# Kernel optimization log

Hardware: AMD Instinct MI355X
Metric: run time of the kernel (lower is better)

Reference implementation:

```python
import jax, jax.numpy as jnp
import numpy as np

N, E, R, B, IN, H, OUT, P = 20000, 320000, 8, 8, 128, 256, 128, 100000
LN_EPS = 1e-5


def _xavier(key, shape):
    fan_in, fan_out = shape[-2], shape[-1]
    lim = float(np.sqrt(6.0 / (fan_in + fan_out)))
    return jax.random.uniform(key, shape, jnp.float32, -lim, lim)


def setup_inputs() -> dict:
    key = jax.random.key(0)
    ks = iter(jax.random.split(key, 64))
    inp = {}
    inp['x'] = jax.random.normal(next(ks), (N, IN), jnp.float32)
    inp['edge_index'] = jax.random.randint(next(ks), (2, E), 0, N, jnp.int32)
    inp['edge_type'] = jax.random.randint(next(ks), (E,), 0, R, jnp.int32)
    inp['gene_pairs'] = jax.random.randint(next(ks), (2, P), 0, N, jnp.int32)
    dims = [(IN, H), (H, H), (H, H), (H, OUT)]  # per-layer (in_ch, out_ch)
    for i, (ic, oc) in enumerate(dims):
        inp[f'basis{i}'] = _xavier(next(ks), (B, ic, oc))
        inp[f'att{i}'] = _xavier(next(ks), (R, B))
        inp[f'root{i}'] = _xavier(next(ks), (ic, oc))
        inp[f'relatt{i}'] = jnp.ones((R,), jnp.float32)
        inp[f'g{i}'] = jnp.ones((oc,), jnp.float32)
        inp[f'b{i}'] = jnp.zeros((oc,), jnp.float32)
    inp['res0'] = _xavier(next(ks), (IN, H))   # in_ch != out_ch at layer 0
    inp['res3'] = _xavier(next(ks), (H, OUT))  # and at layer 3
    # decoder: 3*OUT -> H -> H//2 -> H//4 -> 1
    ddims = [(3 * OUT, H), (H, H // 2), (H // 2, H // 4), (H // 4, 1)]
    for i, (ic, oc) in enumerate(ddims):
        inp[f'dW{i}'] = _xavier(next(ks), (ic, oc))
        inp[f'db{i}'] = jnp.zeros((oc,), jnp.float32)
        if i < 3:
            inp[f'dg{i}'] = jnp.ones((oc,), jnp.float32)
            inp[f'dbb{i}'] = jnp.zeros((oc,), jnp.float32)
    return inp


def _ln(h, g, b):
    m = h.mean(-1, keepdims=True)
    v = ((h - m) ** 2).mean(-1, keepdims=True)
    return (h - m) * jax.lax.rsqrt(v + LN_EPS) * g + b


def _conv(x, src, dst, et, basis, att, root_w, rel_att):
    # W_r = sum_b att[r,b] * B_b ; message = a_{r(e)} * x_src @ W_{r(e)}
    # Since the message is linear, aggregate x_src per (dst, relation) first
    # (segment_sum), then apply the R small GEMMs once - same math, no [E,in,out].
    n, d = x.shape
    weight = jnp.einsum('rb,bio->rio', att, basis)          # [R,in,out]
    a = jax.nn.softmax(rel_att)                              # [R]
    seg = dst.astype(jnp.int32) * R + et.astype(jnp.int32)   # [(node,rel)] segment ids
    agg = jax.ops.segment_sum(x[src], seg, num_segments=n * R).reshape(n, R, d)
    out = jnp.einsum('nri,rio->no', agg, weight * a[:, None, None])
    return out + x @ root_w


def reference(x, edge_index, edge_type, gene_pairs,
              basis0, att0, root0, relatt0, g0, b0, res0,
              basis1, att1, root1, relatt1, g1, b1,
              basis2, att2, root2, relatt2, g2, b2,
              basis3, att3, root3, relatt3, g3, b3, res3,
              dW0, db0, dg0, dbb0, dW1, db1, dg1, dbb1,
              dW2, db2, dg2, dbb2, dW3, db3):
    src, dst = edge_index[0], edge_index[1]
    layers = [
        (basis0, att0, root0, relatt0, g0, b0, res0),
        (basis1, att1, root1, relatt1, g1, b1, None),
        (basis2, att2, root2, relatt2, g2, b2, None),
        (basis3, att3, root3, relatt3, g3, b3, res3),
    ]
    h = x
    for i, (bs, at, rt, ra, g, b, res) in enumerate(layers):
        h_in = h
        h = _conv(h, src, dst, edge_type, bs, at, rt, ra)
        h = _ln(h, g, b)
        h = h + (h_in @ res if res is not None else h_in)
        if i < len(layers) - 1:
            h = jax.nn.gelu(h, approximate=False)
    z = h  # [N, OUT]
    zi, zj = z[gene_pairs[0]], z[gene_pairs[1]]
    pe = jnp.concatenate([zi + zj, zi * zj, jnp.abs(zi - zj)], axis=-1)
    d = jax.nn.gelu(_ln(pe @ dW0 + db0, dg0, dbb0), approximate=False)
    d = jax.nn.gelu(_ln(d @ dW1 + db1, dg1, dbb1), approximate=False)
    d = jax.nn.gelu(_ln(d @ dW2 + db2, dg2, dbb2), approximate=False)
    logits = (d @ dW3 + db3).squeeze(-1)  # [P]
    return logits, z
```

## Files before the change

kernel.cpp:

```cpp
#include <hip/hip_runtime.h>
#include <hip/hip_bf16.h>
#include <math.h>
#include <cstddef>
#include <stdint.h>

#define NN 20000
#define EE 320000
#define RR 8
#define PP 100000
#define NR (NN * RR)

typedef __hip_bfloat16 bf16;
typedef __attribute__((ext_vector_type(8))) short short8;
typedef __attribute__((ext_vector_type(4))) short short4v;
typedef __attribute__((ext_vector_type(4))) float floatx4;

__device__ __forceinline__ float b2f(bf16 v) { return __bfloat162float(v); }
__device__ __forceinline__ bf16 f2b(float v) { return __float2bfloat16(v); }
__device__ __forceinline__ float bits2f(unsigned short u) {
  unsigned int i = ((unsigned int)u) << 16; float f; __builtin_memcpy(&f, &i, 4); return f;
}
__device__ __forceinline__ short f2bits(float f) {
  bf16 h = __float2bfloat16(f); short s; __builtin_memcpy(&s, &h, 2); return s;
}
__device__ __forceinline__ float gelu_f(float x) {
  float t = x * (0.7978845608f + 0.0356774081f * x * x);
  float s = exp2f(-2.885390082f * t);
  return x * __builtin_amdgcn_rcpf(1.f + s);
}
__device__ __forceinline__ void async_copy16(void* lds, const void* g) {
  __builtin_amdgcn_global_load_lds((const __attribute__((address_space(1))) void*)g,
                                   (__attribute__((address_space(3))) void*)lds, 16, 0, 0);
}
__device__ __forceinline__ const short8* frag_at(const bf16* base, int row, int q) {
  return (const short8*)(base + row * 64 + (((q) ^ (row & 7)) << 3));
}
__device__ __forceinline__ const short8* frag256(const bf16* base, int row, int col64, int q) {
  return (const short8*)(base + row * 256 + col64 + (((q) ^ (row & 7)) << 3));
}
__device__ __forceinline__ int idx128(int row, int qg) {
  return row * 128 + ((qg >> 3) << 6) + (((qg & 7) ^ (row & 7)) << 3);
}

__global__ void hist_k(const int* __restrict__ dst, const int* __restrict__ et,
                       int* __restrict__ counts) {
  int e = blockIdx.x * 256 + threadIdx.x;
  if (e >= EE) return;
  atomicAdd(&counts[dst[e] * RR + et[e]], 1);
}

__global__ void scan1_k(const int* __restrict__ counts, int* __restrict__ prefix,
                        int* __restrict__ bsums) {
  __shared__ int tmp[256];
  int i = blockIdx.x * 256 + threadIdx.x;
  int v = counts[i];
  tmp[threadIdx.x] = v; __syncthreads();
  for (int off = 1; off < 256; off <<= 1) {
    int x = (threadIdx.x >= off) ? tmp[threadIdx.x - off] : 0;
    __syncthreads();
    tmp[threadIdx.x] += x;
    __syncthreads();
  }
  prefix[i] = tmp[threadIdx.x] - v;
  if (threadIdx.x == 255) bsums[blockIdx.x] = tmp[255];
}

__global__ void scan2_k(int* __restrict__ bsums, int nb) {
  __shared__ int tmp[256];
  __shared__ int carry;
  if (threadIdx.x == 0) carry = 0;
  __syncthreads();
  for (int base = 0; base < nb; base += 256) {
    int i = base + threadIdx.x;
    int v = (i < nb) ? bsums[i] : 0;
    tmp[threadIdx.x] = v; __syncthreads();
    for (int off = 1; off < 256; off <<= 1) {
      int x = (threadIdx.x >= off) ? tmp[threadIdx.x - off] : 0;
      __syncthreads();
      tmp[threadIdx.x] += x;
      __syncthreads();
    }
    int c = carry;
    if (i < nb) bsums[i] = c + tmp[threadIdx.x] - v;
    __syncthreads();
    if (threadIdx.x == 255) carry = c + tmp[255];
    __syncthreads();
  }
}

__global__ void scan3_k(int* __restrict__ prefix, const int* __restrict__ bsums) {
  int i = blockIdx.x * 256 + threadIdx.x;
  prefix[i] += bsums[blockIdx.x];
}

__global__ void scatter_k(const int* __restrict__ src, const int* __restrict__ dst,
                          const int* __restrict__ et, const int* __restrict__ segstart,
                          int* __restrict__ cursor, int* __restrict__ ssrc) {
  int e = blockIdx.x * 256 + threadIdx.x;
  if (e >= EE) return;
  int s = dst[e] * RR + et[e];
  int pos = atomicAdd(&cursor[s], 1);
  ssrc[segstart[s] + pos] = src[e];
}

__global__ void cvt_bf16_k(const float* __restrict__ in, bf16* __restrict__ out, int n) {
  int i = blockIdx.x * 256 + threadIdx.x;
  if (i < n) out[i] = f2b(in[i]);
}

__global__ void softmax4_k(const float* r0, const float* r1, const float* r2,
                           const float* r3, float* __restrict__ a) {
  if (threadIdx.x == 0) {
    const float* rs[4] = {r0, r1, r2, r3};
    for (int l = 0; l < 4; ++l) {
      float mx = -1e30f;
      for (int i = 0; i < RR; ++i) mx = fmaxf(mx, rs[l][i]);
      float e[RR]; float s = 0.f;
      for (int i = 0; i < RR; ++i) { e[i] = expf(rs[l][i] - mx); s += e[i]; }
      for (int i = 0; i < RR; ++i) a[l * RR + i] = e[i] / s;
    }
  }
}

__global__ void transpose_k(const float* __restrict__ in, bf16* __restrict__ out,
                            int rows, int cols) {
  int idx = blockIdx.x * 256 + threadIdx.x;
  if (idx >= rows * cols) return;
  int r = idx / cols, c = idx - r * cols;
  out[(size_t)c * rows + r] = f2b(in[idx]);
}

__global__ void prep_w_k(const float* __restrict__ basis, const float* __restrict__ att,
                         const float* __restrict__ root, const float* __restrict__ a,
                         bf16* __restrict__ Wt, int ic, int icsh, int oc, int ocsh) {
  int idx = blockIdx.x * 256 + threadIdx.x;
  int cols = 9 * ic;
  if (idx >= cols * oc) return;
  int o = idx & (oc - 1);
  int col = idx >> ocsh;
  int r = col >> icsh;
  int k = col & (ic - 1);
  float val;
  if (r < RR) {
    float acc = 0.f;
    for (int bb = 0; bb < RR; ++bb)
      acc += att[r * RR + bb] * basis[((size_t)bb * ic + k) * oc + o];
    val = a[r] * acc;
  } else {
    val = root[(size_t)k * oc + o];
  }
  Wt[(size_t)o * cols + col] = f2b(val);
}

__global__ __launch_bounds__(256) void aggregate_k(
    const bf16* __restrict__ h, const int* __restrict__ segstart,
    const int* __restrict__ counts, const int* __restrict__ ssrc,
    bf16* __restrict__ agg, int ic, int tpnsh) {
  int tpn = 1 << tpnsh;
  int npb = 256 >> tpnsh;
  int local = threadIdx.x >> tpnsh;
  int n = blockIdx.x * npb + local;
  if (n >= NN) return;
  int cbase = (threadIdx.x & (tpn - 1)) * 8;
  size_t rowoff = (size_t)n * (9 * ic);
  for (int r = 0; r < RR; ++r) {
    int s = n * RR + r;
    int st = segstart[s];
    int cnt = counts[s];
    float a[8] = {0.f, 0.f, 0.f, 0.f, 0.f, 0.f, 0.f, 0.f};
    for (int i = 0; i < cnt; ++i) {
      int src = ssrc[st + i];
      short8 v = *(const short8*)(h + (size_t)src * ic + cbase);
#pragma unroll
      for (int j = 0; j < 8; ++j) a[j] += bits2f((unsigned short)v[j]);
    }
    short8 o;
#pragma unroll
    for (int j = 0; j < 8; ++j) o[j] = f2bits(a[j]);
    *(short8*)(agg + rowoff + r * ic + cbase) = o;
  }
  *(short8*)(agg + rowoff + 8 * ic + cbase) =
      *(const short8*)(h + (size_t)n * ic + cbase);
}

__global__ __launch_bounds__(256) void gemm_f32_k(
    const bf16* __restrict__ A, const bf16* __restrict__ Wt,
    float* __restrict__ Cf, int M, int N, int K, int nb) {
  const int bid = blockIdx.x;
  const int xcd = bid & 7;
  const int slot = bid >> 3;
  const int gidx = slot / nb;
  const int member = slot - gidx * nb;
  const int mb = (M + 127) >> 7;
  const int m = gidx * 8 + xcd;
  if (m >= mb) return;
  const int m0 = m * 128;
  const int n0 = member * 64;

  __shared__ __align__(16) bf16 As[128 * 64];
  __shared__ __align__(16) bf16 Ws[64 * 64];
  const int tid = threadIdx.x;
  const int wave = tid >> 6, lane = tid & 63;
  const int quad = lane >> 4, l16 = lane & 15;
  const int wm = (wave >> 1) * 64, wn = (wave & 1) * 32;
  floatx4 acc[4][2];
#pragma unroll
  for (int i = 0; i < 4; ++i)
#pragma unroll
    for (int j = 0; j < 2; ++j) acc[i][j] = (floatx4){0.f, 0.f, 0.f, 0.f};

  for (int k0 = 0; k0 < K; k0 += 64) {
#pragma unroll
    for (int q = 0; q < 4; ++q) {
      int c0 = (wave * 4 + q) * 1024;
      int row = (c0 >> 7) + (lane >> 3);
      int grow = m0 + row; if (grow >= M) grow = M - 1;
      int ch = (lane & 7) ^ (row & 7);
      async_copy16((char*)As + c0, A + (size_t)grow * K + k0 + ch * 8);
    }
#pragma unroll
    for (int q = 0; q < 2; ++q) {
      int c0 = (wave * 2 + q) * 1024;
      int row = (c0 >> 7) + (lane >> 3);
      int ch = (lane & 7) ^ (row & 7);
      async_copy16((char*)Ws + c0, Wt + (size_t)(n0 + row) * K + k0 + ch * 8);
    }
    __syncthreads();
#pragma unroll
    for (int kk = 0; kk < 64; kk += 32) {
      int qb = (kk >> 3) + quad;
      short8 b0 = *frag_at(Ws, wn + l16, qb);
      short8 b1 = *frag_at(Ws, wn + 16 + l16, qb);
#pragma unroll
      for (int i = 0; i < 4; ++i) {
        short8 a = *frag_at(As, wm + i * 16 + l16, qb);
        acc[i][0] = __builtin_amdgcn_mfma_f32_16x16x32_bf16(a, b0, acc[i][0], 0, 0, 0);
        acc[i][1] = __builtin_amdgcn_mfma_f32_16x16x32_bf16(a, b1, acc[i][1], 0, 0, 0);
      }
    }
    __syncthreads();
  }
#pragma unroll
  for (int i = 0; i < 4; ++i)
#pragma unroll
    for (int j = 0; j < 2; ++j)
#pragma unroll
      for (int r = 0; r < 4; ++r) {
        int row = m0 + wm + i * 16 + quad * 4 + r;
        int col = n0 + wn + j * 16 + l16;
        if (row < M) Cf[(size_t)row * N + col] = acc[i][j][r];
      }
}

__global__ __launch_bounds__(256) void gemm_plain_k(
    const bf16* __restrict__ A, const bf16* __restrict__ Wt,
    bf16* __restrict__ Cb, int M, int N, int K) {
  __shared__ __align__(16) bf16 As[64 * 64];
  __shared__ __align__(16) bf16 Ws[64 * 64];
  const int m0 = blockIdx.y * 64;
  const int n0 = blockIdx.x * 64;
  const int tid = threadIdx.x;
  const int wave = tid >> 6, lane = tid & 63;
  const int quad = lane >> 4, l16 = lane & 15;
  const int wm = (wave >> 1) * 32, wn = (wave & 1) * 32;
  floatx4 acc00 = {0.f, 0.f, 0.f, 0.f};
  floatx4 acc01 = acc00, acc10 = acc00, acc11 = acc00;

  for (int k0 = 0; k0 < K; k0 += 64) {
#pragma unroll
    for (int q = 0; q < 2; ++q) {
      int c0 = (wave * 2 + q) * 1024;
      int row = (c0 >> 7) + (lane >> 3);
      int grow = m0 + row; if (grow >= M) grow = M - 1;
      int ch = (lane & 7) ^ (row & 7);
      async_copy16((char*)As + c0, A + (size_t)grow * K + k0 + ch * 8);
    }
#pragma unroll
    for (int q = 0; q < 2; ++q) {
      int c0 = (wave * 2 + q) * 1024;
      int row = (c0 >> 7) + (lane >> 3);
      int ch = (lane & 7) ^ (row & 7);
      async_copy16((char*)Ws + c0, Wt + (size_t)(n0 + row) * K + k0 + ch * 8);
    }
    __syncthreads();
#pragma unroll
    for (int kk = 0; kk < 64; kk += 32) {
      int qb = (kk >> 3) + quad;
      short8 a0 = *frag_at(As, wm + l16, qb);
      short8 a1 = *frag_at(As, wm + 16 + l16, qb);
      short8 b0 = *frag_at(Ws, wn + l16, qb);
      short8 b1 = *frag_at(Ws, wn + 16 + l16, qb);
      acc00 = __builtin_amdgcn_mfma_f32_16x16x32_bf16(a0, b0, acc00, 0, 0, 0);
      acc01 = __builtin_amdgcn_mfma_f32_16x16x32_bf16(a0, b1, acc01, 0, 0, 0);
      acc10 = __builtin_amdgcn_mfma_f32_16x16x32_bf16(a1, b0, acc10, 0, 0, 0);
      acc11 = __builtin_amdgcn_mfma_f32_16x16x32_bf16(a1, b1, acc11, 0, 0, 0);
    }
    __syncthreads();
  }
  floatx4 accs[2][2] = {{acc00, acc01}, {acc10, acc11}};
#pragma unroll
  for (int i = 0; i < 2; ++i)
#pragma unroll
    for (int j = 0; j < 2; ++j)
#pragma unroll
      for (int r = 0; r < 4; ++r) {
        int row = m0 + wm + i * 16 + quad * 4 + r;
        int col = n0 + wn + j * 16 + l16;
        if (row < M) Cb[(size_t)row * N + col] = f2b(accs[i][j][r]);
      }
}

__global__ __launch_bounds__(256) void ln_conv_k(
    const float* __restrict__ conv, const bf16* __restrict__ res,
    const float* __restrict__ g, const float* __restrict__ b,
    bf16* __restrict__ out, float* __restrict__ zout, int oc, int do_gelu) {
  int wave = threadIdx.x >> 6, lane = threadIdx.x & 63;
  int row = blockIdx.x * 4 + wave;
  if (row >= NN) return;
  int ne = oc >> 6;
  float v[4];
  float s = 0.f, s2 = 0.f;
  for (int i = 0; i < ne; ++i) {
    v[i] = conv[(size_t)row * oc + i * 64 + lane];
    s += v[i]; s2 += v[i] * v[i];
  }
  for (int off = 32; off; off >>= 1) { s += __shfl_xor(s, off); s2 += __shfl_xor(s2, off); }
  float m = s / oc;
  float var = s2 / oc - m * m;
  float rs = rsqrtf(var + 1e-5f);
  for (int i = 0; i < ne; ++i) {
    int c = i * 64 + lane;
    float y = (v[i] - m) * rs * g[c] + b[c];
    y += b2f(res[(size_t)row * oc + c]);
    if (zout) zout[(size_t)row * oc + c] = y;
    if (do_gelu) y = gelu_f(y);
    out[(size_t)row * oc + c] = f2b(y);
  }
}

__global__ __launch_bounds__(256) void gemm_pe_k(
    const bf16* __restrict__ z, const int* __restrict__ pairs,
    const bf16* __restrict__ WBT, const bf16* __restrict__ WCT,
    bf16* __restrict__ P0) {
  const int bid = blockIdx.x;
  const int xcd = bid & 7;
  const int slot = bid >> 3;
  const int gidx = slot >> 2;
  const int member = slot & 3;
  const int mb = (PP + 127) >> 7;
  const int m = gidx * 8 + xcd;
  if (m >= mb) return;
  const int m0 = m * 128;
  const int n0 = member * 64;

  __shared__ __align__(16) bf16 PEs[128 * 64];
  __shared__ __align__(16) bf16 Ws[64 * 64];
  const int tid = threadIdx.x;
  const int wave = tid >> 6, lane = tid & 63;
  const int quad = lane >> 4, l16 = lane & 15;
  const int wm = (wave >> 1) * 64, wn = (wave & 1) * 32;

  const int prow = tid >> 1;
  const int colq = (tid & 1) * 32;
  int pp = m0 + prow; if (pp >= PP) pp = PP - 1;
  const bf16* zi = z + (size_t)pairs[pp] * 128;
  const bf16* zj = z + (size_t)pairs[PP + pp] * 128;

  floatx4 acc[4][2];
#pragma unroll
  for (int i = 0; i < 4; ++i)
#pragma unroll
    for (int j = 0; j < 2; ++j) acc[i][j] = (floatx4){0.f, 0.f, 0.f, 0.f};

#pragma unroll
  for (int kwi = 0; kwi < 2; ++kwi) {
    const int kw = kwi * 64;
    short8 va[4], vb[4];
#pragma unroll
    for (int c8 = 0; c8 < 4; ++c8) {
      va[c8] = *(const short8*)(zi + kw + colq + c8 * 8);
      vb[c8] = *(const short8*)(zj + kw + colq + c8 * 8);
    }
#pragma unroll
    for (int op = 0; op < 2; ++op) {
      const bf16* W = (op == 0) ? WBT : WCT;
#pragma unroll
      for (int q = 0; q < 2; ++q) {
        int c0 = q * 4096 + wave * 1024;
        int row = (c0 >> 7) + (lane >> 3);
        int ch = (lane & 7) ^ (row & 7);
        async_copy16((char*)Ws + c0, W + (size_t)(n0 + row) * 128 + kw + ch * 8);
      }
#pragma unroll
      for (int c8 = 0; c8 < 4; ++c8) {
        short8 o;
#pragma unroll
        for (int jj = 0; jj < 8; ++jj) {
          float fa = bits2f((unsigned short)va[c8][jj]);
          float fb = bits2f((unsigned short)vb[c8][jj]);
          float v = (op == 0) ? (fa * fb) : fabsf(fa - fb);
          o[jj] = f2bits(v);
        }
        int q = (tid & 1) * 4 + c8;
        *(short8*)(PEs + prow * 64 + ((q ^ (prow & 7)) << 3)) = o;
      }
      __syncthreads();
#pragma unroll
      for (int kk = 0; kk < 64; kk += 32) {
        int qb = (kk >> 3) + quad;
        short8 b0 = *frag_at(Ws, wn + l16, qb);
        short8 b1 = *frag_at(Ws, wn + 16 + l16, qb);
#pragma unroll
        for (int i = 0; i < 4; ++i) {
          short8 a = *frag_at(PEs, wm + i * 16 + l16, qb);
          acc[i][0] = __builtin_amdgcn_mfma_f32_16x16x32_bf16(a, b0, acc[i][0], 0, 0, 0);
          acc[i][1] = __builtin_amdgcn_mfma_f32_16x16x32_bf16(a, b1, acc[i][1], 0, 0, 0);
        }
      }
      __syncthreads();
    }
  }

#pragma unroll
  for (int i = 0; i < 4; ++i)
#pragma unroll
    for (int j = 0; j < 2; ++j)
#pragma unroll
      for (int r = 0; r < 4; ++r) {
        int row = m0 + wm + i * 16 + quad * 4 + r;
        int col = n0 + wn + j * 16 + l16;
        if (row < PP) P0[(size_t)row * 256 + col] = f2b(acc[i][j][r]);
      }
}

__global__ __launch_bounds__(256) void ln_d0_k(bf16* __restrict__ D0,
                                               const int* __restrict__ pairs,
                                               const bf16* __restrict__ ZA,
                                               const float* __restrict__ db0,
                                               const float* __restrict__ g,
                                               const float* __restrict__ b) {
  int wave = threadIdx.x >> 6, lane = threadIdx.x & 63;
  int row = blockIdx.x * 4 + wave;
  if (row >= PP) return;
  int gi = pairs[row], gj = pairs[PP + row];
  bf16* p = D0 + (size_t)row * 256 + lane * 4;
  short4v xv = *(const short4v*)p;
  short4v av = *(const short4v*)(ZA + (size_t)gi * 256 + lane * 4);
  short4v bv = *(const short4v*)(ZA + (size_t)gj * 256 + lane * 4);
  float v[4];
  float s = 0.f, s2 = 0.f;
#pragma unroll
  for (int k = 0; k < 4; ++k) {
    v[k] = bits2f((unsigned short)xv[k]) + bits2f((unsigned short)av[k]) +
           bits2f((unsigned short)bv[k]) + db0[lane * 4 + k];
    s += v[k]; s2 += v[k] * v[k];
  }
  for (int off = 32; off; off >>= 1) { s += __shfl_xor(s, off); s2 += __shfl_xor(s2, off); }
  float m = s / 256.f;
  float var = s2 / 256.f - m * m;
  float rs = rsqrtf(var + 1e-5f);
  short4v ov;
#pragma unroll
  for (int k = 0; k < 4; ++k) {
    int c = lane * 4 + k;
    float y = (v[k] - m) * rs * g[c] + b[c];
    ov[k] = f2bits(gelu_f(y));
  }
  *(short4v*)p = ov;
}

__global__ __launch_bounds__(256) void lngemm1_k(
    const bf16* __restrict__ D0, const bf16* __restrict__ W1t,
    const float* __restrict__ bias, bf16* __restrict__ P1, int M) {
  __shared__ __align__(16) bf16 As[64 * 256];
  __shared__ __align__(16) bf16 Ws[128 * 64];
  const int tid = threadIdx.x;
  const int wave = tid >> 6, lane = tid & 63;
  const int quad = lane >> 4, l16 = lane & 15;
  const int wr = (wave >> 1) * 32;
  const int wc = (wave & 1) * 64;
  const int m0 = blockIdx.x * 64;

  {
    const int srow = tid >> 2;
    const int q4 = tid & 3;
    int grow = m0 + srow; if (grow >= M) grow = M - 1;
    const bf16* src = D0 + (size_t)grow * 256 + q4 * 64;
#pragma unroll
    for (int c8 = 0; c8 < 8; ++c8) {
      short8 o = *(const short8*)(src + c8 * 8);
      *(short8*)(As + srow * 256 + q4 * 64 + ((c8 ^ (srow & 7)) << 3)) = o;
    }
  }

  floatx4 acc[2][4];
#pragma unroll
  for (int i = 0; i < 2; ++i)
#pragma unroll
    for (int j = 0; j < 4; ++j) acc[i][j] = (floatx4){0.f, 0.f, 0.f, 0.f};

  for (int kc = 0; kc < 4; ++kc) {
#pragma unroll
    for (int q = 0; q < 4; ++q) {
      int c0 = q * 4096 + wave * 1024;
      int row = (c0 >> 7) + (lane >> 3);
      int ch = (lane & 7) ^ (row & 7);
      async_copy16((char*)Ws + c0, W1t + (size_t)row * 256 + kc * 64 + ch * 8);
    }
    __syncthreads();
#pragma unroll
    for (int kk = 0; kk < 64; kk += 32) {
      int qb = (kk >> 3) + quad;
      short8 a0 = *frag256(As, wr + l16, kc * 64, qb);
      short8 a1 = *frag256(As, wr + 16 + l16, kc * 64, qb);
#pragma unroll
      for (int j = 0; j < 4; ++j) {
        short8 bb = *frag_at(Ws, wc + j * 16 + l16, qb);
        acc[0][j] = __builtin_amdgcn_mfma_f32_16x16x32_bf16(a0, bb, acc[0][j], 0, 0, 0);
        acc[1][j] = __builtin_amdgcn_mfma_f32_16x16x32_bf16(a1, bb, acc[1][j], 0, 0, 0);
      }
    }
    __syncthreads();
  }

#pragma unroll
  for (int i = 0; i < 2; ++i)
#pragma unroll
    for (int r = 0; r < 4; ++r) {
      int row = wr + i * 16 + quad * 4 + r;
      int grow = m0 + row;
      if (grow >= M) continue;
#pragma unroll
      for (int j = 0; j < 4; ++j) {
        int col = wc + j * 16 + l16;
        P1[(size_t)grow * 128 + col] = f2b(acc[i][j][r] + bias[col]);
      }
    }
}

__global__ __launch_bounds__(256) void lngemm2_k(
    const bf16* __restrict__ P1, const bf16* __restrict__ W2t,
    const float* __restrict__ g, const float* __restrict__ b,
    const float* __restrict__ bias, bf16* __restrict__ P2, int M) {
  __shared__ __align__(16) bf16 As[64 * 128];
  __shared__ __align__(16) bf16 Ws[64 * 64];
  const int tid = threadIdx.x;
  const int wave = tid >> 6, lane = tid & 63;
  const int quad = lane >> 4, l16 = lane & 15;
  const int m0 = blockIdx.x * 64;

  {
    const int srow = tid >> 2;
    const int q4 = tid & 3;
    int grow = m0 + srow; if (grow >= M) grow = M - 1;
    const bf16* src = P1 + (size_t)grow * 128 + q4 * 32;
    float v[32];
    float s = 0.f, s2 = 0.f;
#pragma unroll
    for (int c8 = 0; c8 < 4; ++c8) {
      short8 x = *(const short8*)(src + c8 * 8);
#pragma unroll
      for (int jj = 0; jj < 8; ++jj) {
        float f = bits2f((unsigned short)x[jj]);
        v[c8 * 8 + jj] = f; s += f; s2 += f * f;
      }
    }
    s += __shfl_xor(s, 1); s2 += __shfl_xor(s2, 1);
    s += __shfl_xor(s, 2); s2 += __shfl_xor(s2, 2);
    float mean = s / 128.f;
    float var = s2 / 128.f - mean * mean;
    float rs = rsqrtf(var + 1e-5f);
#pragma unroll
    for (int c8 = 0; c8 < 4; ++c8) {
      short8 o;
#pragma unroll
      for (int jj = 0; jj < 8; ++jj) {
        int col = q4 * 32 + c8 * 8 + jj;
        float y = (v[c8 * 8 + jj] - mean) * rs * g[col] + b[col];
        o[jj] = f2bits(gelu_f(y));
      }
      *(short8*)(As + idx128(srow, q4 * 4 + c8)) = o;
    }
  }

  floatx4 acc[4];
#pragma unroll
  for (int j = 0; j < 4; ++j) acc[j] = (floatx4){0.f, 0.f, 0.f, 0.f};

  for (int kc = 0; kc < 2; ++kc) {
#pragma unroll
    for (int q = 0; q < 2; ++q) {
      int c0 = q * 4096 + wave * 1024;
      int row = (c0 >> 7) + (lane >> 3);
      int ch = (lane & 7) ^ (row & 7);
      async_copy16((char*)Ws + c0, W2t + (size_t)row * 128 + kc * 64 + ch * 8);
    }
    __syncthreads();
#pragma unroll
    for (int kk = 0; kk < 64; kk += 32) {
      int qb = (kk >> 3) + quad;
      short8 a = *(const short8*)(As + idx128(wave * 16 + l16, kc * 8 + qb));
#pragma unroll
      for (int j = 0; j < 4; ++j) {
        short8 bb = *frag_at(Ws, j * 16 + l16, qb);
        acc[j] = __builtin_amdgcn_mfma_f32_16x16x32_bf16(a, bb, acc[j], 0, 0, 0);
      }
    }
    __syncthreads();
  }

#pragma unroll
  for (int r = 0; r < 4; ++r) {
    int row = wave * 16 + quad * 4 + r;
    int grow = m0 + row;
    if (grow >= M) continue;
#pragma unroll
    for (int j = 0; j < 4; ++j) {
      int col = j * 16 + l16;
      P2[(size_t)grow * 64 + col] = f2b(acc[j][r] + bias[col]);
    }
  }
}

__global__ __launch_bounds__(256) void logits_k(const bf16* __restrict__ P2,
                                                const float* __restrict__ g,
                                                const float* __restrict__ b,
                                                const float* __restrict__ w3,
                                                const float* __restrict__ b3,
                                                float* __restrict__ out) {
  int wave = threadIdx.x >> 6, lane = threadIdx.x & 63;
  int p = blockIdx.x * 4 + wave;
  if (p >= PP) return;
  float v = b2f(P2[(size_t)p * 64 + lane]);
  float s = v, s2 = v * v;
  for (int off = 32; off; off >>= 1) { s += __shfl_xor(s, off); s2 += __shfl_xor(s2, off); }
  float m = s / 64.f;
  float var = s2 / 64.f - m * m;
  float rs = rsqrtf(var + 1e-5f);
  float y = gelu_f((v - m) * rs * g[lane] + b[lane]);
  float t = y * w3[lane];
  for (int off = 32; off; off >>= 1) t += __shfl_xor(t, off);
  if (lane == 0) out[p] = t + b3[0];
}

extern "C" void kernel_launch(void* const* d_in, const int* in_sizes, int n_in,
                              void* d_out, int out_size, void* d_ws, size_t ws_size,
                              hipStream_t stream) {
  auto cdiv = [](int a, int b) { return (a + b - 1) / b; };

  const float* x = (const float*)d_in[0];
  const int* ei = (const int*)d_in[1];
  const int* et = (const int*)d_in[2];
  const int* gp = (const int*)d_in[3];
  const float *basis[4], *att[4], *root[4], *relatt[4], *gln[4], *bln[4];
  for (int l = 0; l < 4; ++l) {
    basis[l]  = (const float*)d_in[4 + 6 * l];
    att[l]    = (const float*)d_in[5 + 6 * l];
    root[l]   = (const float*)d_in[6 + 6 * l];
    relatt[l] = (const float*)d_in[7 + 6 * l];
    gln[l]    = (const float*)d_in[8 + 6 * l];
    bln[l]    = (const float*)d_in[9 + 6 * l];
  }
  const float* res0 = (const float*)d_in[28];
  const float* res3 = (const float*)d_in[29];
  const float* dW0 = (const float*)d_in[30]; const float* db0 = (const float*)d_in[31];
  const float* dg0 = (const float*)d_in[32]; const float* dbb0 = (const float*)d_in[33];
  const float* dW1 = (const float*)d_in[34]; const float* db1 = (const float*)d_in[35];
  const float* dg1 = (const float*)d_in[36]; const float* dbb1 = (const float*)d_in[37];
  const float* dW2 = (const float*)d_in[38]; const float* db2 = (const float*)d_in[39];
  const float* dg2 = (const float*)d_in[40]; const float* dbb2 = (const float*)d_in[41];
  const float* dW3 = (const float*)d_in[42]; const float* db3 = (const float*)d_in[43];

  char* base = (char*)d_ws;
  size_t off = 0;
  auto alloc = [&](size_t bytes) -> char* {
    char* p = base + off;
    off += (bytes + 255) & ~(size_t)255;
    return p;
  };
  bf16* X16 = (bf16*)alloc((size_t)NN * 128 * 2);
  bf16* HA  = (bf16*)alloc((size_t)NN * 256 * 2);
  bf16* HB  = (bf16*)alloc((size_t)NN * 256 * 2);
  bf16* RESB = (bf16*)alloc((size_t)NN * 256 * 2);
  bf16* ZA   = (bf16*)alloc((size_t)NN * 256 * 2);
  float* CONV = (float*)alloc((size_t)NN * 256 * 4);
  bf16* WT    = (bf16*)alloc((size_t)589824 * 2);
  bf16* RES0T = (bf16*)alloc((size_t)32768 * 2);
  bf16* RES3T = (bf16*)alloc((size_t)32768 * 2);
  bf16* WAT   = (bf16*)alloc((size_t)32768 * 2);
  bf16* WBT   = (bf16*)alloc((size_t)32768 * 2);
  bf16* WCT   = (bf16*)alloc((size_t)32768 * 2);
  bf16* DW1T  = (bf16*)alloc((size_t)32768 * 2);
  bf16* DW2T  = (bf16*)alloc((size_t)8192 * 2);
  float* ASOFT = (float*)alloc(32 * 4);
  int* COUNTS = (int*)alloc((size_t)NR * 4);
  int* SEG    = (int*)alloc((size_t)NR * 4);
  int* CUR    = (int*)alloc((size_t)NR * 4);
  int* BS     = (int*)alloc(1024 * 4);
  int* SSRC   = (int*)alloc((size_t)EE * 4);
  char* BIG = alloc(93000000);
  bf16* AGG = (bf16*)BIG;
  bf16* D0  = (bf16*)BIG;
  bf16* P1  = (bf16*)alloc((size_t)PP * 128 * 2);
  bf16* P2  = (bf16*)alloc((size_t)PP * 64 * 2);
  (void)ws_size; (void)in_sizes; (void)n_in; (void)out_size;

  float* out_logits = (float*)d_out;
  float* out_z = (float*)d_out + PP;

  hipMemsetAsync(COUNTS, 0, (size_t)NR * 4, stream);
  hipMemsetAsync(CUR, 0, (size_t)NR * 4, stream);
  hist_k<<<cdiv(EE, 256), 256, 0, stream>>>(ei + EE, et, COUNTS);
  scan1_k<<<NR / 256, 256, 0, stream>>>(COUNTS, SEG, BS);
  scan2_k<<<1, 256, 0, stream>>>(BS, NR / 256);
  scan3_k<<<NR / 256, 256, 0, stream>>>(SEG, BS);
  scatter_k<<<cdiv(EE, 256), 256, 0, stream>>>(ei, ei + EE, et, SEG, CUR, SSRC);

  cvt_bf16_k<<<cdiv(NN * 128, 256), 256, 0, stream>>>(x, X16, NN * 128);
  softmax4_k<<<1, 64, 0, stream>>>(relatt[0], relatt[1], relatt[2], relatt[3], ASOFT);
  transpose_k<<<cdiv(128 * 256, 256), 256, 0, stream>>>(res0, RES0T, 128, 256);
  transpose_k<<<cdiv(256 * 128, 256), 256, 0, stream>>>(res3, RES3T, 256, 128);
  transpose_k<<<cdiv(128 * 256, 256), 256, 0, stream>>>(dW0, WAT, 128, 256);
  transpose_k<<<cdiv(128 * 256, 256), 256, 0, stream>>>(dW0 + 128 * 256, WBT, 128, 256);
  transpose_k<<<cdiv(128 * 256, 256), 256, 0, stream>>>(dW0 + 256 * 256, WCT, 128, 256);
  transpose_k<<<cdiv(256 * 128, 256), 256, 0, stream>>>(dW1, DW1T, 256, 128);
  transpose_k<<<cdiv(128 * 64, 256), 256, 0, stream>>>(dW2, DW2T, 128, 64);

  const int mb = cdiv(NN, 128);
  const int swzP4 = 8 * cdiv(mb, 8) * 4;
  const int swzP2 = 8 * cdiv(mb, 8) * 2;

  prep_w_k<<<cdiv(9 * 128 * 256, 256), 256, 0, stream>>>(basis[0], att[0], root[0], ASOFT + 0, WT, 128, 7, 256, 8);
  aggregate_k<<<cdiv(NN, 16), 256, 0, stream>>>(X16, SEG, COUNTS, SSRC, AGG, 128, 4);
  gemm_plain_k<<<dim3(4, cdiv(NN, 64)), 256, 0, stream>>>(X16, RES0T, RESB, NN, 256, 128);
  gemm_f32_k<<<swzP4, 256, 0, stream>>>(AGG, WT, CONV, NN, 256, 1152, 4);
  ln_conv_k<<<cdiv(NN, 4), 256, 0, stream>>>(CONV, RESB, gln[0], bln[0], HA, nullptr, 256, 1);

  prep_w_k<<<cdiv(9 * 256 * 256, 256), 256, 0, stream>>>(basis[1], att[1], root[1], ASOFT + 8, WT, 256, 8, 256, 8);
  aggregate_k<<<cdiv(NN, 8), 256, 0, stream>>>(HA, SEG, COUNTS, SSRC, AGG, 256, 5);
  gemm_f32_k<<<swzP4, 256, 0, stream>>>(AGG, WT, CONV, NN, 256, 2304, 4);
  ln_conv_k<<<cdiv(NN, 4), 256, 0, stream>>>(CONV, HA, gln[1], bln[1], HB, nullptr, 256, 1);

  prep_w_k<<<cdiv(9 * 256 * 256, 256), 256, 0, stream>>>(basis[2], att[2], root[2], ASOFT + 16, WT, 256, 8, 256, 8);
  aggregate_k<<<cdiv(NN, 8), 256, 0, stream>>>(HB, SEG, COUNTS, SSRC, AGG, 256, 5);
  gemm_f32_k<<<swzP4, 256, 0, stream>>>(AGG, WT, CONV, NN, 256, 2304, 4);
  ln_conv_k<<<cdiv(NN, 4), 256, 0, stream>>>(CONV, HB, gln[2], bln[2], HA, nullptr, 256, 1);

  prep_w_k<<<cdiv(9 * 256 * 128, 256), 256, 0, stream>>>(basis[3], att[3], root[3], ASOFT + 24, WT, 256, 8, 128, 7);
  aggregate_k<<<cdiv(NN, 8), 256, 0, stream>>>(HA, SEG, COUNTS, SSRC, AGG, 256, 5);
  gemm_plain_k<<<dim3(2, cdiv(NN, 64)), 256, 0, stream>>>(HA, RES3T, RESB, NN, 128, 256);
  gemm_f32_k<<<swzP2, 256, 0, stream>>>(AGG, WT, CONV, NN, 128, 2304, 2);
  ln_conv_k<<<cdiv(NN, 4), 256, 0, stream>>>(CONV, RESB, gln[3], bln[3], HB, out_z, 128, 0);

  gemm_plain_k<<<dim3(4, cdiv(NN, 64)), 256, 0, stream>>>(HB, WAT, ZA, NN, 256, 128);
  const int pb = cdiv(PP, 128);
  const int swzPE = 8 * cdiv(pb, 8) * 4;
  gemm_pe_k<<<swzPE, 256, 0, stream>>>(HB, gp, WBT, WCT, D0);
  ln_d0_k<<<cdiv(PP, 4), 256, 0, stream>>>(D0, gp, ZA, db0, dg0, dbb0);
  lngemm1_k<<<cdiv(PP, 64), 256, 0, stream>>>(D0, DW1T, db1, P1, PP);
  lngemm2_k<<<cdiv(PP, 4 * 16), 256, 0, stream>>>(P1, DW2T, dg1, dbb1, db2, P2, PP);
  logits_k<<<cdiv(PP, 4), 256, 0, stream>>>(P2, dg2, dbb2, dW3, db3, out_logits);
}
```

Baseline: 762.0 us.

## Fuse decoder layer-0 LayerNorm into GEMM1 load and interleave aggregation relations

The separate ln_d0_k pass is removed. Its bias add, ZA gathers, LayerNorm and GELU now run while lngemm1_k loads its A tile, with four threads per row reducing the statistics through shuffles. This avoids a full read and write of the 100000x256 D0 buffer and one kernel launch, at the cost of 64 floats of register state per thread. The aggregate kernel also loads segment starts and counts as vectors and walks two relations at once, unrolled by two, so more independent gathers are in flight.

```diff
diff --git a/kernel.cpp b/kernel.cpp
--- a/kernel.cpp
+++ b/kernel.cpp
@@ -14,6 +14,7 @@
 typedef __attribute__((ext_vector_type(8))) short short8;
 typedef __attribute__((ext_vector_type(4))) short short4v;
 typedef __attribute__((ext_vector_type(4))) float floatx4;
+typedef __attribute__((ext_vector_type(4))) int intx4;
 
 __device__ __forceinline__ float b2f(bf16 v) { return __bfloat162float(v); }
 __device__ __forceinline__ bf16 f2b(float v) { return __float2bfloat16(v); }
@@ -163,21 +164,69 @@
   if (n >= NN) return;
   int cbase = (threadIdx.x & (tpn - 1)) * 8;
   size_t rowoff = (size_t)n * (9 * ic);
-  for (int r = 0; r < RR; ++r) {
-    int s = n * RR + r;
-    int st = segstart[s];
-    int cnt = counts[s];
-    float a[8] = {0.f, 0.f, 0.f, 0.f, 0.f, 0.f, 0.f, 0.f};
-    for (int i = 0; i < cnt; ++i) {
-      int src = ssrc[st + i];
-      short8 v = *(const short8*)(h + (size_t)src * ic + cbase);
-#pragma unroll
-      for (int j = 0; j < 8; ++j) a[j] += bits2f((unsigned short)v[j]);
-    }
-    short8 o;
-#pragma unroll
-    for (int j = 0; j < 8; ++j) o[j] = f2bits(a[j]);
-    *(short8*)(agg + rowoff + r * ic + cbase) = o;
+  const bf16* hc = h + cbase;
+
+  intx4 stv0 = *(const intx4*)(segstart + n * RR);
+  intx4 stv1 = *(const intx4*)(segstart + n * RR + 4);
+  intx4 ctv0 = *(const intx4*)(counts + n * RR);
+  intx4 ctv1 = *(const intx4*)(counts + n * RR + 4);
+  int sts[8] = {stv0[0], stv0[1], stv0[2], stv0[3], stv1[0], stv1[1], stv1[2], stv1[3]};
+  int cts[8] = {ctv0[0], ctv0[1], ctv0[2], ctv0[3], ctv1[0], ctv1[1], ctv1[2], ctv1[3]};
+
+#pragma unroll
+  for (int rp = 0; rp < 4; ++rp) {
+    const int stA = sts[rp],     cA = cts[rp];
+    const int stB = sts[rp + 4], cB = cts[rp + 4];
+    float aA[8] = {0.f, 0.f, 0.f, 0.f, 0.f, 0.f, 0.f, 0.f};
+    float aB[8] = {0.f, 0.f, 0.f, 0.f, 0.f, 0.f, 0.f, 0.f};
+    int iA = 0, iB = 0;
+    while (iA + 2 <= cA && iB + 2 <= cB) {
+      int sA0 = ssrc[stA + iA], sA1 = ssrc[stA + iA + 1];
+      int sB0 = ssrc[stB + iB], sB1 = ssrc[stB + iB + 1];
+      short8 vA0 = *(const short8*)(hc + (size_t)sA0 * ic);
+      short8 vA1 = *(const short8*)(hc + (size_t)sA1 * ic);
+      short8 vB0 = *(const short8*)(hc + (size_t)sB0 * ic);
+      short8 vB1 = *(const short8*)(hc + (size_t)sB1 * ic);
+#pragma unroll
+      for (int j = 0; j < 8; ++j) {
+        aA[j] += bits2f((unsigned short)vA0[j]) + bits2f((unsigned short)vA1[j]);
+        aB[j] += bits2f((unsigned short)vB0[j]) + bits2f((unsigned short)vB1[j]);
+      }
+      iA += 2; iB += 2;
+    }
+    for (; iA + 2 <= cA; iA += 2) {
+      int s0 = ssrc[stA + iA], s1 = ssrc[stA + iA + 1];
+      short8 v0 = *(const short8*)(hc + (size_t)s0 * ic);
+      short8 v1 = *(const short8*)(hc + (size_t)s1 * ic);
+#pragma unroll
+      for (int j = 0; j < 8; ++j)
+        aA[j] += bits2f((unsigned short)v0[j]) + bits2f((unsigned short)v1[j]);
+    }
+    if (iA < cA) {
+      int s0 = ssrc[stA + iA];
+      short8 v0 = *(const short8*)(hc + (size_t)s0 * ic);
+#pragma unroll
+      for (int j = 0; j < 8; ++j) aA[j] += bits2f((unsigned short)v0[j]);
+    }
+    for (; iB + 2 <= cB; iB += 2) {
+      int s0 = ssrc[stB + iB], s1 = ssrc[stB + iB + 1];
+      short8 v0 = *(const short8*)(hc + (size_t)s0 * ic);
+      short8 v1 = *(const short8*)(hc + (size_t)s1 * ic);
+#pragma unroll
+      for (int j = 0; j < 8; ++j)
+        aB[j] += bits2f((unsigned short)v0[j]) + bits2f((unsigned short)v1[j]);
+    }
+    if (iB < cB) {
+      int s0 = ssrc[stB + iB];
+      short8 v0 = *(const short8*)(hc + (size_t)s0 * ic);
+#pragma unroll
+      for (int j = 0; j < 8; ++j) aB[j] += bits2f((unsigned short)v0[j]);
+    }
+    short8 oA, oB;
+#pragma unroll
+    for (int j = 0; j < 8; ++j) { oA[j] = f2bits(aA[j]); oB[j] = f2bits(aB[j]); }
+    *(short8*)(agg + rowoff + rp * ic + cbase) = oA;
+    *(short8*)(agg + rowoff + (rp + 4) * ic + cbase) = oB;
   }
   *(short8*)(agg + rowoff + 8 * ic + cbase) =
       *(const short8*)(h + (size_t)n * ic + cbase);
@@ -433,44 +482,11 @@
       }
 }
 
-__global__ __launch_bounds__(256) void ln_d0_k(bf16* __restrict__ D0,
-                                               const int* __restrict__ pairs,
-                                               const bf16* __restrict__ ZA,
-                                               const float* __restrict__ db0,
-                                               const float* __restrict__ g,
-                                               const float* __restrict__ b) {
-  int wave = threadIdx.x >> 6, lane = threadIdx.x & 63;
-  int row = blockIdx.x * 4 + wave;
-  if (row >= PP) return;
-  int gi = pairs[row], gj = pairs[PP + row];
-  bf16* p = D0 + (size_t)row * 256 + lane * 4;
-  short4v xv = *(const short4v*)p;
-  short4v av = *(const short4v*)(ZA + (size_t)gi * 256 + lane * 4);
-  short4v bv = *(const short4v*)(ZA + (size_t)gj * 256 + lane * 4);
-  float v[4];
-  float s = 0.f, s2 = 0.f;
-#pragma unroll
-  for (int k = 0; k < 4; ++k) {
-    v[k] = bits2f((unsigned short)xv[k]) + bits2f((unsigned short)av[k]) +
-           bits2f((unsigned short)bv[k]) + db0[lane * 4 + k];
-    s += v[k]; s2 += v[k] * v[k];
-  }
-  for (int off = 32; off; off >>= 1) { s += __shfl_xor(s, off); s2 += __shfl_xor(s2, off); }
-  float m = s / 256.f;
-  float var = s2 / 256.f - m * m;
-  float rs = rsqrtf(var + 1e-5f);
-  short4v ov;
-#pragma unroll
-  for (int k = 0; k < 4; ++k) {
-    int c = lane * 4 + k;
-    float y = (v[k] - m) * rs * g[c] + b[c];
-    ov[k] = f2bits(gelu_f(y));
-  }
-  *(short4v*)p = ov;
-}
-
 __global__ __launch_bounds__(256) void lngemm1_k(
-    const bf16* __restrict__ D0, const bf16* __restrict__ W1t,
+    const bf16* __restrict__ P0, const int* __restrict__ pairs,
+    const bf16* __restrict__ ZA, const float* __restrict__ db0,
+    const float* __restrict__ g0, const float* __restrict__ b0,
+    const bf16* __restrict__ W1t,
     const float* __restrict__ bias, bf16* __restrict__ P1, int M) {
   __shared__ __align__(16) bf16 As[64 * 256];
   __shared__ __align__(16) bf16 Ws[128 * 64];
@@ -485,10 +501,39 @@
     const int srow = tid >> 2;
     const int q4 = tid & 3;
     int grow = m0 + srow; if (grow >= M) grow = M - 1;
-    const bf16* src = D0 + (size_t)grow * 256 + q4 * 64;
+    int gi = pairs[grow], gj = pairs[PP + grow];
+    const bf16* p0 = P0 + (size_t)grow * 256 + q4 * 64;
+    const bf16* za = ZA + (size_t)gi * 256 + q4 * 64;
+    const bf16* zb = ZA + (size_t)gj * 256 + q4 * 64;
+    float v[64];
+    float s = 0.f, s2 = 0.f;
 #pragma unroll
     for (int c8 = 0; c8 < 8; ++c8) {
-      short8 o = *(const short8*)(src + c8 * 8);
+      short8 xp = *(const short8*)(p0 + c8 * 8);
+      short8 xa = *(const short8*)(za + c8 * 8);
+      short8 xb = *(const short8*)(zb + c8 * 8);
+#pragma unroll
+      for (int jj = 0; jj < 8; ++jj) {
+        int col = q4 * 64 + c8 * 8 + jj;
+        float f = bits2f((unsigned short)xp[jj]) + bits2f((unsigned short)xa[jj]) +
+                  bits2f((unsigned short)xb[jj]) + db0[col];
+        v[c8 * 8 + jj] = f; s += f; s2 += f * f;
+      }
+    }
+    s += __shfl_xor(s, 1); s2 += __shfl_xor(s2, 1);
+    s += __shfl_xor(s, 2); s2 += __shfl_xor(s2, 2);
+    float mean = s / 256.f;
+    float var = s2 / 256.f - mean * mean;
+    float rs = rsqrtf(var + 1e-5f);
+#pragma unroll
+    for (int c8 = 0; c8 < 8; ++c8) {
+      short8 o;
+#pragma unroll
+      for (int jj = 0; jj < 8; ++jj) {
+        int col = q4 * 64 + c8 * 8 + jj;
+        float y = (v[c8 * 8 + jj] - mean) * rs * g0[col] + b0[col];
+        o[jj] = f2bits(gelu_f(y));
+      }
       *(short8*)(As + srow * 256 + q4 * 64 + ((c8 ^ (srow & 7)) << 3)) = o;
     }
   }
@@ -700,7 +745,7 @@
   int* SSRC   = (int*)alloc((size_t)EE * 4);
   char* BIG = alloc(93000000);
   bf16* AGG = (bf16*)BIG;
-  bf16* D0  = (bf16*)BIG;
+  bf16* P0  = (bf16*)BIG;
   bf16* P1  = (bf16*)alloc((size_t)PP * 128 * 2);
   bf16* P2  = (bf16*)alloc((size_t)PP * 64 * 2);
   (void)ws_size; (void)in_sizes; (void)n_in; (void)out_size;
@@ -755,9 +800,8 @@
   gemm_plain_k<<<dim3(4, cdiv(NN, 64)), 256, 0, stream>>>(HB, WAT, ZA, NN, 256, 128);
   const int pb = cdiv(PP, 128);
   const int swzPE = 8 * cdiv(pb, 8) * 4;
-  gemm_pe_k<<<swzPE, 256, 0, stream>>>(HB, gp, WBT, WCT, D0);
-  ln_d0_k<<<cdiv(PP, 4), 256, 0, stream>>>(D0, gp, ZA, db0, dg0, dbb0);
-  lngemm1_k<<<cdiv(PP, 64), 256, 0, stream>>>(D0, DW1T, db1, P1, PP);
+  gemm_pe_k<<<swzPE, 256, 0, stream>>>(HB, gp, WBT, WCT, P0);
+  lngemm1_k<<<cdiv(PP, 64), 256, 0, stream>>>(P0, gp, ZA, db0, dg0, dbb0, DW1T, db1, P1, PP);
   lngemm2_k<<<cdiv(PP, 4 * 16), 256, 0, stream>>>(P1, DW2T, dg1, dbb1, db2, P2, PP);
   logits_k<<<cdiv(PP, 4), 256, 0, stream>>>(P2, dg2, dbb2, dW3, db3, out_logits);
 }
```

Result: faster. 739.8 us (-2.9%).
